# Kernel optimization log

Measured on AMD Instinct MI355X. Metric: run time of the kernel, lower is better.

The kernel has to match this reference:

```python
import jax, jax.numpy as jnp
import numpy as np
from jax import lax

B, S, D, N, K = 4, 8192, 128, 2, 3
G = N + 1  # n_order + 1 projection groups
EPS_L1 = 1e-8


def _theta(d):
    # RoPE inverse frequencies: 10000^{-2i/d}
    return 1.0 / (10000.0 ** (jnp.arange(d // 2, dtype=jnp.float32) * 2.0 / d))


def _rope(x, pos, theta):
    # x: (B,S,D), pos: (B,S) int -> dimension-wise 2x2 rotations
    ang = pos[..., None].astype(jnp.float32) * theta  # (B,S,D/2)
    c, s = jnp.cos(ang), jnp.sin(ang)
    xe, xo = x[..., 0::2], x[..., 1::2]
    return jnp.stack([xe * c - xo * s, xe * s + xo * c], axis=-1).reshape(x.shape)


def _layernorm(x, g, b, eps=1e-5):
    mu = jnp.mean(x, axis=-1, keepdims=True)
    var = jnp.var(x, axis=-1, keepdims=True)
    return (x - mu) / jnp.sqrt(var + eps) * g + b


def _fft_long_conv(v, h):
    # torch norm='forward': rfft divides by n, irfft does not -> circular conv / (2L)
    L = v.shape[-1]
    n = 2 * L
    V = jnp.fft.rfft(v, n=n, norm='forward')
    H = jnp.fft.rfft(h, n=n, norm='forward')
    return jnp.fft.irfft(V * H, n=n, norm='forward')[..., :L]


def setup_inputs() -> dict:
    key = jax.random.key(0)
    ks = jax.random.split(key, 8)
    sc = lambda fan_in: (2.0 / fan_in) ** 0.5
    return {
        'embeddings': jax.random.normal(ks[0], (B, S, D), dtype=jnp.float32),
        'W_proj': jax.random.normal(ks[1], (D, G * D), dtype=jnp.float32) * sc(D),
        'conv_w': jax.random.normal(ks[2], (G * D, 1, K), dtype=jnp.float32) * sc(K),
        'conv_b': jnp.zeros((G * D,), dtype=jnp.float32),
        'W1': jax.random.normal(ks[3], (D, D), dtype=jnp.float32) * sc(D),
        'b1': jnp.zeros((D,), dtype=jnp.float32),
        'ln_g': jnp.ones((D,), dtype=jnp.float32),
        'ln_b': jnp.zeros((D,), dtype=jnp.float32),
        'W2': jax.random.normal(ks[4], (D, N * D), dtype=jnp.float32) * sc(D),
        'b2': jnp.zeros((N * D,), dtype=jnp.float32),
        'ff_scale': jnp.ones((1, 1, N * D), dtype=jnp.float32),
        'out_proj': jax.random.normal(ks[5], (D, D), dtype=jnp.float32) * sc(D),
        'B_param': jax.random.normal(ks[6], (N, 1, D, 1), dtype=jnp.float32) * sc(D),
        'positions': (jnp.arange(B * S, dtype=jnp.int32).reshape(B, S) % S),
    }


def reference(embeddings, W_proj, conv_w, conv_b, W1, b1, ln_g, ln_b, W2, b2,
              ff_scale, out_proj, B_param, positions):
    theta = _theta(D)
    # --- HyenaProjection: dense proj + fully-depthwise short conv ---
    x = embeddings @ W_proj                      # (B,S,G*D)
    xc = jnp.transpose(x, (0, 2, 1))             # (B,G*D,S)
    z = lax.conv_general_dilated(
        xc, conv_w, (1,), [(K // 2, K // 2)],
        dimension_numbers=('NCH', 'OIH', 'NCH'),
        feature_group_count=G * D) + conv_b[None, :, None]
    # faithful to torch: (B,S,G*D) row-major reshape into (B,D,G,S)
    z = jnp.transpose(z, (0, 2, 1)).reshape(B, D, G, S)
    z_list = [z[:, :, i, :] for i in range(G)]   # each (B,D,S)
    # --- HyenaFilter: RoPE + FFN + L1 normalization over emb dim ---
    t = _rope(embeddings, positions, theta)
    hmid = jax.nn.gelu(_layernorm(t @ W1 + b1, ln_g, ln_b), approximate=False)
    h_hat = (hmid @ W2 + b2) * ff_scale          # (B,S,N*D)
    h_hat = jnp.transpose(h_hat.reshape(B, S, N, D), (0, 2, 3, 1))  # (B,N,D,S)
    h_hat = h_hat / (jnp.sum(jnp.abs(h_hat), axis=-2, keepdims=True) + EPS_L1)
    # --- Hyena recurrence with FFT long conv ---
    v = z_list[-1]
    for i in range(N):
        v = z_list[i] * (_fft_long_conv(v, h_hat[:, i]) + B_param[i] * v)
    out = jnp.transpose(v, (0, 2, 1)) @ out_proj  # (B,S,D)
    return out
```

## Files before the change

kernel.cpp:

```cpp
#include <hip/hip_runtime.h>
#include <hip/hip_bf16.h>
#include <cstdint>

#define BB 4
#define SS 8192
#define DD 128

#define N_EMB  4194304
#define N_WP   49152
#define N_CW   1152
#define N_CB   384
#define N_W1   16384
#define N_B1   128
#define N_LNG  128
#define N_LNB  128
#define N_W2   32768
#define N_B2   256
#define N_FFS  256
#define N_WO   16384
#define N_BP   256
#define N_FINP 4311680

__device__ __forceinline__ void bfsplit(float v, unsigned short& h, unsigned short& l)
{
    __hip_bfloat16 hb = __float2bfloat16(v);
    float hf = __bfloat162float(hb);
    __hip_bfloat16 lb = __float2bfloat16(v - hf);
    h = *(unsigned short*)&hb;
    l = *(unsigned short*)&lb;
}

struct SrcPtrs { const void* p[13]; };

__global__ __launch_bounds__(256) void k_convert(
    SrcPtrs sp, float* __restrict__ dst,
    unsigned short* __restrict__ embh, unsigned short* __restrict__ embl,
    unsigned short* __restrict__ wpth, unsigned short* __restrict__ wptl)
{
    static const int sizes[13] = {N_EMB, N_WP, N_CW, N_CB, N_W1, N_B1, N_LNG,
                                  N_LNB, N_W2, N_B2, N_FFS, N_WO, N_BP};
    const unsigned probe = *(const unsigned*)sp.p[6];
    const bool isbf = (probe != 0x3F800000u);
    const int gid = blockIdx.x * 256 + threadIdx.x;
    const int stride = gridDim.x * 256;
    int off = 0;
    for (int seg = 0; seg < 13; ++seg) {
        const int n = sizes[seg];
        float* d = dst + off;
        if (isbf) {
            const unsigned short* s = (const unsigned short*)sp.p[seg];
            for (int i = gid; i < n; i += stride) {
                float v = __uint_as_float(((unsigned)s[i]) << 16);
                d[i] = v;
                if (seg == 0) { unsigned short h, l; bfsplit(v, h, l); embh[i] = h; embl[i] = l; }
            }
        } else {
            const float* s = (const float*)sp.p[seg];
            for (int i = gid; i < n; i += stride) {
                float v = s[i];
                d[i] = v;
                if (seg == 0) { unsigned short h, l; bfsplit(v, h, l); embh[i] = h; embl[i] = l; }
            }
        }
        off += n;
    }
    for (int i = gid; i < N_WP; i += stride) {
        int n = i >> 7, k = i & 127;
        float v;
        if (isbf) v = __uint_as_float(((unsigned)((const unsigned short*)sp.p[1])[k * 384 + n]) << 16);
        else      v = ((const float*)sp.p[1])[k * 384 + n];
        unsigned short h, l; bfsplit(v, h, l);
        wpth[i] = h; wptl[i] = l;
    }
}

#define PCROWS 112

__global__ __launch_bounds__(512) void k_projconv(
    const unsigned short* __restrict__ embh,
    const unsigned short* __restrict__ embl,
    const unsigned short* __restrict__ wpth,
    const unsigned short* __restrict__ wptl,
    const float* __restrict__ cw,
    const float* __restrict__ cb,
    float* __restrict__ zbuf)
{
    typedef short bf16x8 __attribute__((ext_vector_type(8)));
    typedef float f32x4 __attribute__((ext_vector_type(4)));
    __shared__ float xs[128][68];

    const int b    = blockIdx.y;
    const int s0   = blockIdx.x * PCROWS;
    const int t    = threadIdx.x;
    const int wv   = t >> 6;
    const int lane = t & 63;
    const int m    = lane & 15;
    const int q    = lane >> 4;

    bf16x8 Ah[4], Al[4];
    {
        int sx  = s0 - 8 + 16 * wv + m;
        int sxc = min(max(sx, 0), SS - 1);
        const size_t rowoff = ((size_t)b * SS + sxc) * DD;
        #pragma unroll
        for (int kt = 0; kt < 4; ++kt) {
            int k0 = kt * 32 + q * 8;
            Ah[kt] = *(const bf16x8*)(embh + rowoff + k0);
            Al[kt] = *(const bf16x8*)(embl + rowoff + k0);
        }
    }

    for (int nc = 0; nc < 6; ++nc) {
        #pragma unroll
        for (int nt = 0; nt < 4; ++nt) {
            int n = nc * 64 + nt * 16 + m;
            const size_t noff = (size_t)n * DD;
            f32x4 acc = {0.f, 0.f, 0.f, 0.f};
            #pragma unroll
            for (int kt = 0; kt < 4; ++kt) {
                int k0 = kt * 32 + q * 8;
                bf16x8 Bh = *(const bf16x8*)(wpth + noff + k0);
                bf16x8 Bl = *(const bf16x8*)(wptl + noff + k0);
                acc = __builtin_amdgcn_mfma_f32_16x16x32_bf16(Ah[kt], Bh, acc, 0, 0, 0);
                acc = __builtin_amdgcn_mfma_f32_16x16x32_bf16(Ah[kt], Bl, acc, 0, 0, 0);
                acc = __builtin_amdgcn_mfma_f32_16x16x32_bf16(Al[kt], Bh, acc, 0, 0, 0);
            }
            #pragma unroll
            for (int rg = 0; rg < 4; ++rg)
                xs[16 * wv + 4 * q + rg][nt * 16 + m] = acc[rg];
        }
        __syncthreads();
        {
            int c = t & 63, rg = t >> 6;
            int ch = nc * 64 + c;
            float w0 = cw[ch * 3 + 0], w1 = cw[ch * 3 + 1], w2 = cw[ch * 3 + 2];
            float bias = cb[ch];
            #pragma unroll
            for (int i = 0; i < 14; ++i) {
                int r = rg + 8 * i;
                int s = s0 + r;
                if (s < SS) {
                    float x0 = (s > 0)      ? xs[r + 7][c] : 0.f;
                    float x1 = xs[r + 8][c];
                    float x2 = (s < SS - 1) ? xs[r + 9][c] : 0.f;
                    zbuf[((size_t)b * SS + s) * 384 + ch] = x0 * w0 + x1 * w1 + x2 * w2 + bias;
                }
            }
        }
        __syncthreads();
    }
}

__global__ __launch_bounds__(256) void k_mlp(
    const float* __restrict__ emb,
    const int* __restrict__ positions,
    const float* __restrict__ W1,
    const float* __restrict__ b1,
    const float* __restrict__ ln_g,
    const float* __restrict__ ln_b,
    const float* __restrict__ W2,
    const float* __restrict__ b2,
    const float* __restrict__ ffs,
    float* __restrict__ hhat)
{
    const int b  = blockIdx.y;
    const int s0 = blockIdx.x * 16;
    const int t  = threadIdx.x;
    __shared__ float tls[16][128];
    __shared__ float hls[16][128];
    __shared__ float hh[16][257];
    __shared__ float rstat[16][2];

    for (int idx = t; idx < 16 * 64; idx += 256) {
        int r = idx >> 6, i = idx & 63;
        int s = s0 + r;
        const float2 p = ((const float2*)(emb + ((size_t)b * SS + s) * DD))[i];
        float xe = p.x, xo = p.y;
        float pos = (float)positions[(size_t)b * SS + s];
        float th = exp2f((float)i * (-13.287712379549449f / 64.0f));
        float ang = pos * th;
        float sn, cs;
        sincosf(ang, &sn, &cs);
        tls[r][2 * i]     = xe * cs - xo * sn;
        tls[r][2 * i + 1] = xe * sn + xo * cs;
    }
    __syncthreads();

    {
        const int jc = t & 127;
        const int rbase = t >> 7;
        float bias = b1[jc];
        float acc[8];
        #pragma unroll
        for (int ri = 0; ri < 8; ++ri) acc[ri] = bias;
        for (int k = 0; k < 128; ++k) {
            float wv = W1[k * 128 + jc];
            #pragma unroll
            for (int ri = 0; ri < 8; ++ri)
                acc[ri] += tls[rbase + 2 * ri][k] * wv;
        }
        #pragma unroll
        for (int ri = 0; ri < 8; ++ri) hls[rbase + 2 * ri][jc] = acc[ri];
    }
    __syncthreads();

    {
        const int wave = t >> 6, lane = t & 63;
        for (int r = wave; r < 16; r += 4) {
            float x0 = hls[r][lane], x1 = hls[r][lane + 64];
            float sum = x0 + x1, ssq = x0 * x0 + x1 * x1;
            #pragma unroll
            for (int off = 32; off > 0; off >>= 1) {
                sum += __shfl_xor(sum, off);
                ssq += __shfl_xor(ssq, off);
            }
            float mu  = sum * (1.0f / 128.0f);
            float var = ssq * (1.0f / 128.0f) - mu * mu;
            float inv = rsqrtf(var + 1e-5f);
            float y0 = (x0 - mu) * inv * ln_g[lane]      + ln_b[lane];
            float y1 = (x1 - mu) * inv * ln_g[lane + 64] + ln_b[lane + 64];
            hls[r][lane]      = y0 * 0.5f * (1.0f + erff(y0 * 0.70710678118654752f));
            hls[r][lane + 64] = y1 * 0.5f * (1.0f + erff(y1 * 0.70710678118654752f));
        }
    }
    __syncthreads();

    {
        const int jc = t;
        float acc[16];
        #pragma unroll
        for (int ri = 0; ri < 16; ++ri) acc[ri] = 0.f;
        for (int k = 0; k < 128; ++k) {
            float wv = W2[k * 256 + jc];
            #pragma unroll
            for (int ri = 0; ri < 16; ++ri)
                acc[ri] += hls[ri][k] * wv;
        }
        float bias = b2[jc];
        float fsc  = ffs[jc];
        #pragma unroll
        for (int ri = 0; ri < 16; ++ri)
            hh[ri][jc] = (acc[ri] + bias) * fsc;
    }
    __syncthreads();

    {
        const int wave = t >> 6, lane = t & 63;
        for (int g = wave; g < 32; g += 4) {
            int r = g >> 1, n = g & 1;
            float a = fabsf(hh[r][n * 128 + lane]) + fabsf(hh[r][n * 128 + lane + 64]);
            #pragma unroll
            for (int off = 32; off > 0; off >>= 1) a += __shfl_xor(a, off);
            if (lane == 0) rstat[r][n] = 1.0f / (a + 1e-8f);
        }
    }
    __syncthreads();

    for (int idx = t; idx < 16 * 256; idx += 256) {
        int nd = idx >> 4, rr = idx & 15;
        int n = nd >> 7;
        float val = hh[rr][nd] * rstat[rr][n];
        hhat[((size_t)(b * 2 + n) * 128 + (nd & 127)) * SS + (s0 + rr)] = val;
    }
}

__device__ __forceinline__ int SK(int x) { return x + (x >> 5); }

__global__ __launch_bounds__(1024) void k_fftconv(
    const float* __restrict__ zbuf,
    const float* __restrict__ hhat,
    const float* __restrict__ Bp,
    float* __restrict__ vout)
{
    const int d = blockIdx.x;
    const int b = blockIdx.y;
    const int t = threadIdx.x;
    __shared__ float lre[4224];
    __shared__ float lim[4224];
    __shared__ float2 twF[1280];

    const float c8 = 0.923879532511287f, s8 = 0.382683432365090f, c4 = 0.707106781186548f;

    {
        const int lhs_c[5] = {9, 7, 5, 3, 1};
        for (int idx = t; idx < 1280; idx += 1024) {
            int si = idx >> 8, jj = idx & 255;
            float sn, cs;
            sincospif((float)jj * (-1.0f / (float)(1 << lhs_c[si])), &sn, &cs);
            twF[idx] = make_float2(cs, sn);
        }
    }

    const float* zb = zbuf + (size_t)b * (SS * 384);
    const float* v0 = zb + ((size_t)d * 3 + 2) * SS;
    float vr[8];
    #pragma unroll
    for (int j = 0; j < 8; ++j) vr[j] = v0[t + j * 1024];

    float cre[16], cim[16];
    const float sc = 1.0f / 536870912.0f;
    const int blk = t >> 8, w = t & 255;
    __syncthreads();

    for (int it = 0; it < 2; ++it) {
        const float* hp = hhat + (((size_t)b * 2 + it) * 128 + d) * SS;
        #pragma unroll
        for (int j = 0; j < 8; ++j) { cre[j] = vr[j]; cim[j] = hp[t + j * 1024]; }

        {
            float W0i, W0r; sincospif((float)t * (-1.0f / 8192.0f), &W0i, &W0r);
            const float wjr[4] = {1.f, c8, c4, s8};
            const float wji[4] = {0.f, -s8, -c4, -c8};
            #pragma unroll
            for (int j = 0; j < 4; ++j) {
                float Wr = W0r * wjr[j] - W0i * wji[j];
                float Wi = W0r * wji[j] + W0i * wjr[j];
                float W2r = Wr * Wr - Wi * Wi, W2i = 2.f * Wr * Wi;
                float W3r = W2r * Wr - W2i * Wi, W3i = W2r * Wi + W2i * Wr;
                float a0r = cre[j], a0i = cim[j], a1r = cre[j + 4], a1i = cim[j + 4];
                cre[j] = a0r + a1r; cim[j] = a0i + a1i;
                float dr = a0r - a1r, di = a0i - a1i;
                cre[j + 4] = W2r * dr - W2i * di; cim[j + 4] = W2r * di + W2i * dr;
                float e2r = a0r + a1i, e2i = a0i - a1r;
                cre[j + 8] = Wr * e2r - Wi * e2i; cim[j + 8] = Wr * e2i + Wi * e2r;
                float e3r = a0r - a1i, e3i = a0i + a1r;
                cre[j + 12] = W3r * e3r - W3i * e3i; cim[j + 12] = W3r * e3i + W3i * e3r;
            }
        }
        {
            float Wi, Wr; sincospif((float)t * (-1.0f / 2048.0f), &Wi, &Wr);
            float W2r = Wr * Wr - Wi * Wi, W2i = 2.f * Wr * Wi;
            float W3r = W2r * Wr - W2i * Wi, W3i = W2r * Wi + W2i * Wr;
            #pragma unroll
            for (int g = 0; g < 16; g += 4) {
                float a0r = cre[g], a0i = cim[g], a1r = cre[g + 1], a1i = cim[g + 1];
                float a2r = cre[g + 2], a2i = cim[g + 2], a3r = cre[g + 3], a3i = cim[g + 3];
                float s02r = a0r + a2r, s02i = a0i + a2i, d02r = a0r - a2r, d02i = a0i - a2i;
                float s13r = a1r + a3r, s13i = a1i + a3i, d13r = a1r - a3r, d13i = a1i - a3i;
                cre[g] = s02r + s13r; cim[g] = s02i + s13i;
                float u1r = s02r - s13r, u1i = s02i - s13i;
                cre[g + 1] = W2r * u1r - W2i * u1i; cim[g + 1] = W2r * u1i + W2i * u1r;
                float e2r = d02r + d13i, e2i = d02i - d13r;
                cre[g + 2] = Wr * e2r - Wi * e2i; cim[g + 2] = Wr * e2i + Wi * e2r;
                float e3r = d02r - d13i, e3i = d02i + d13r;
                cre[g + 3] = W3r * e3r - W3i * e3i; cim[g + 3] = W3r * e3i + W3i * e3r;
            }
        }
        #pragma unroll
        for (int p = 0; p < 4; ++p) {
            #pragma unroll
            for (int q = 0; q < 4; ++q) {
                int a = SK(q * 1024 + t);
                lre[a] = cre[4 * p + q]; lim[a] = cim[4 * p + q];
            }
            __syncthreads();
            const int lhs_c[5] = {9, 7, 5, 3, 1};
            #pragma unroll
            for (int si = 0; si < 5; ++si) {
                const int lh = lhs_c[si];
                const int hh = 1 << lh, h2 = hh >> 1;
                const int jj = w & (h2 - 1);
                const int i0 = blk * 1024 + ((w >> (lh - 1)) << (lh + 1)) + jj;
                const float2 wv = twF[si * 256 + jj];
                const float Wr = wv.x, Wi = wv.y;
                const int p0 = SK(i0), p1 = SK(i0 + h2), p2 = SK(i0 + hh), p3 = SK(i0 + hh + h2);
                float a0r = lre[p0], a0i = lim[p0];
                float a1r = lre[p1], a1i = lim[p1];
                float a2r = lre[p2], a2i = lim[p2];
                float a3r = lre[p3], a3i = lim[p3];
                float W2r = Wr * Wr - Wi * Wi, W2i = 2.f * Wr * Wi;
                float W3r = W2r * Wr - W2i * Wi, W3i = W2r * Wi + W2i * Wr;
                float s02r = a0r + a2r, s02i = a0i + a2i, d02r = a0r - a2r, d02i = a0i - a2i;
                float s13r = a1r + a3r, s13i = a1i + a3i, d13r = a1r - a3r, d13i = a1i - a3i;
                lre[p0] = s02r + s13r; lim[p0] = s02i + s13i;
                float u1r = s02r - s13r, u1i = s02i - s13i;
                lre[p1] = W2r * u1r - W2i * u1i; lim[p1] = W2r * u1i + W2i * u1r;
                float e2r = d02r + d13i, e2i = d02i - d13r;
                lre[p2] = Wr * e2r - Wi * e2i; lim[p2] = Wr * e2i + Wi * e2r;
                float e3r = d02r - d13i, e3i = d02i + d13r;
                lre[p3] = W3r * e3r - W3i * e3i; lim[p3] = W3r * e3i + W3i * e3r;
                __syncthreads();
            }
            #pragma unroll
            for (int q = 0; q < 4; ++q) {
                int a = SK(q * 1024 + t);
                cre[4 * p + q] = lre[a]; cim[4 * p + q] = lim[a];
            }
            __syncthreads();
        }

        #pragma unroll
        for (int j = 0; j < 16; ++j) {
            float Cr = cre[j], Ci = cim[j];
            cre[j] = (Cr * Cr - Ci * Ci) * sc;
            cim[j] = 2.0f * Cr * Ci * sc;
        }

        #pragma unroll
        for (int p = 0; p < 4; ++p) {
            #pragma unroll
            for (int q = 0; q < 4; ++q) {
                int a = SK(q * 1024 + t);
                lre[a] = cre[4 * p + q]; lim[a] = cim[4 * p + q];
            }
            __syncthreads();
            const int lqs_c[5] = {0, 2, 4, 6, 8};
            #pragma unroll
            for (int si = 0; si < 5; ++si) {
                const int lq = lqs_c[si];
                const int qv = 1 << lq;
                const int jj = w & (qv - 1);
                const int i0 = blk * 1024 + ((w >> lq) << (lq + 2)) + jj;
                const float2 wv = twF[(4 - si) * 256 + jj];
                const float Wbr = wv.x, Wbi = -wv.y;
                const int p0 = SK(i0), p1 = SK(i0 + qv), p2 = SK(i0 + 2 * qv), p3 = SK(i0 + 3 * qv);
                float a0r = lre[p0], a0i = lim[p0];
                float a1r = lre[p1], a1i = lim[p1];
                float a2r = lre[p2], a2i = lim[p2];
                float a3r = lre[p3], a3i = lim[p3];
                float War = Wbr * Wbr - Wbi * Wbi, Wai = 2.f * Wbr * Wbi;
                float t1r = War * a1r - Wai * a1i, t1i = War * a1i + Wai * a1r;
                float b0r = a0r + t1r, b0i = a0i + t1i, b1r = a0r - t1r, b1i = a0i - t1i;
                float t3r = War * a3r - Wai * a3i, t3i = War * a3i + Wai * a3r;
                float b2r = a2r + t3r, b2i = a2i + t3i, b3r = a2r - t3r, b3i = a2i - t3i;
                float u2r = Wbr * b2r - Wbi * b2i, u2i = Wbr * b2i + Wbi * b2r;
                lre[p0] = b0r + u2r; lim[p0] = b0i + u2i;
                lre[p2] = b0r - u2r; lim[p2] = b0i - u2i;
                float u3r = -Wbi * b3r - Wbr * b3i, u3i = Wbr * b3r - Wbi * b3i;
                lre[p1] = b1r + u3r; lim[p1] = b1i + u3i;
                lre[p3] = b1r - u3r; lim[p3] = b1i - u3i;
                __syncthreads();
            }
            #pragma unroll
            for (int q = 0; q < 4; ++q) {
                int a = SK(q * 1024 + t);
                cre[4 * p + q] = lre[a]; cim[4 * p + q] = lim[a];
            }
            __syncthreads();
        }
        {
            float Wbi, Wbr; sincospif((float)t * (1.0f / 2048.0f), &Wbi, &Wbr);
            float War = Wbr * Wbr - Wbi * Wbi, Wai = 2.f * Wbr * Wbi;
            #pragma unroll
            for (int g = 0; g < 16; g += 4) {
                float a0r = cre[g], a0i = cim[g], a1r = cre[g + 1], a1i = cim[g + 1];
                float a2r = cre[g + 2], a2i = cim[g + 2], a3r = cre[g + 3], a3i = cim[g + 3];
                float t1r = War * a1r - Wai * a1i, t1i = War * a1i + Wai * a1r;
                float b0r = a0r + t1r, b0i = a0i + t1i, b1r = a0r - t1r, b1i = a0i - t1i;
                float t3r = War * a3r - Wai * a3i, t3i = War * a3i + Wai * a3r;
                float b2r = a2r + t3r, b2i = a2i + t3i, b3r = a2r - t3r, b3i = a2i - t3i;
                float u2r = Wbr * b2r - Wbi * b2i, u2i = Wbr * b2i + Wbi * b2r;
                cre[g] = b0r + u2r; cim[g] = b0i + u2i;
                cre[g + 2] = b0r - u2r; cim[g + 2] = b0i - u2i;
                float u3r = -Wbi * b3r - Wbr * b3i, u3i = Wbr * b3r - Wbi * b3i;
                cre[g + 1] = b1r + u3r; cim[g + 1] = b1i + u3i;
                cre[g + 3] = b1r - u3r; cim[g + 3] = b1i - u3i;
            }
        }
        {
            float Bi, Br; sincospif((float)t * (1.0f / 8192.0f), &Bi, &Br);
            const float bjr[4] = {1.f, c8, c4, s8};
            const float bji[4] = {0.f, s8, c4, c8};
            #pragma unroll
            for (int j = 0; j < 4; ++j) {
                float Wbr = Br * bjr[j] - Bi * bji[j];
                float Wbi = Br * bji[j] + Bi * bjr[j];
                float War = Wbr * Wbr - Wbi * Wbi, Wai = 2.f * Wbr * Wbi;
                float a0r = cre[j], a0i = cim[j], a1r = cre[j + 4], a1i = cim[j + 4];
                float a2r = cre[j + 8], a2i = cim[j + 8], a3r = cre[j + 12], a3i = cim[j + 12];
                float t1r = War * a1r - Wai * a1i, t1i = War * a1i + Wai * a1r;
                float b0r = a0r + t1r, b0i = a0i + t1i, b1r = a0r - t1r, b1i = a0i - t1i;
                float t3r = War * a3r - Wai * a3i, t3i = War * a3i + Wai * a3r;
                float b2r = a2r + t3r, b2i = a2i + t3i, b3r = a2r - t3r, b3i = a2i - t3i;
                float u2r = Wbr * b2r - Wbi * b2i, u2i = Wbr * b2i + Wbi * b2r;
                cre[j] = b0r + u2r; cim[j] = b0i + u2i;
                cre[j + 8] = b0r - u2r; cim[j + 8] = b0i - u2i;
                float u3r = -Wbi * b3r - Wbr * b3i, u3i = Wbr * b3r - Wbi * b3i;
                cre[j + 4] = b1r + u3r; cim[j + 4] = b1i + u3i;
                cre[j + 12] = b1r - u3r; cim[j + 12] = b1i - u3i;
            }
        }

        const float* zi = zb + ((size_t)d * 3 + it) * SS;
        const float bpv = Bp[it * 128 + d];
        #pragma unroll
        for (int j = 0; j < 8; ++j) {
            float zz = zi[t + j * 1024];
            vr[j] = zz * (cim[j] + bpv * vr[j]);
        }
        __syncthreads();
    }

    float* vo = vout + ((size_t)b * 128 + d) * SS;
    #pragma unroll
    for (int j = 0; j < 8; ++j) vo[t + j * 1024] = vr[j];
}

__global__ __launch_bounds__(256) void k_outproj(
    const float* __restrict__ vbuf,
    const float* __restrict__ Wo,
    const unsigned* __restrict__ probe,
    void* __restrict__ outv)
{
    const int b  = blockIdx.y;
    const int s0 = blockIdx.x * 64;
    const int t  = threadIdx.x;
    __shared__ float vt[128 * 64];
    for (int idx = t; idx < 8192; idx += 256) {
        int dd = idx >> 6, sl = idx & 63;
        vt[idx] = vbuf[((size_t)b * 128 + dd) * SS + s0 + sl];
    }
    const bool isbf = (*probe != 0x3F800000u);
    __syncthreads();
    {
        const int jc  = t & 127;
        const int slb = t >> 7;
        float acc[32];
        #pragma unroll
        for (int ii = 0; ii < 32; ++ii) acc[ii] = 0.f;
        for (int k = 0; k < 128; ++k) {
            float wv = Wo[k * 128 + jc];
            #pragma unroll
            for (int ii = 0; ii < 32; ++ii)
                acc[ii] += vt[k * 64 + slb + 2 * ii] * wv;
        }
        if (isbf) {
            __hip_bfloat16* out = (__hip_bfloat16*)outv;
            #pragma unroll
            for (int ii = 0; ii < 32; ++ii)
                out[((size_t)b * SS + s0 + slb + 2 * ii) * DD + jc] = __float2bfloat16(acc[ii]);
        } else {
            float* out = (float*)outv;
            #pragma unroll
            for (int ii = 0; ii < 32; ++ii)
                out[((size_t)b * SS + s0 + slb + 2 * ii) * DD + jc] = acc[ii];
        }
    }
}

extern "C" void kernel_launch(void* const* d_in, const int* in_sizes, int n_in,
                              void* d_out, int out_size, void* d_ws, size_t ws_size,
                              hipStream_t stream)
{
    (void)in_sizes; (void)n_in; (void)out_size; (void)ws_size;
    const int* positions = (const int*)d_in[13];

    float* finp = (float*)d_ws;
    float* zbuf = finp + N_FINP;
    float* hhat = zbuf + (size_t)BB * SS * 384;
    float* vbuf = hhat + (size_t)BB * 2 * 128 * SS;
    unsigned short* embh = (unsigned short*)(vbuf + (size_t)BB * 128 * SS);
    unsigned short* embl = embh + N_EMB;
    unsigned short* wpth = embl + N_EMB;
    unsigned short* wptl = wpth + N_WP;

    const float* emb = finp;
    const float* Wp  = emb + N_EMB;
    const float* cw  = Wp  + N_WP;
    const float* cb  = cw  + N_CW;
    const float* W1  = cb  + N_CB;
    const float* b1  = W1  + N_W1;
    const float* lng = b1  + N_B1;
    const float* lnb = lng + N_LNG;
    const float* W2  = lnb + N_LNB;
    const float* b2  = W2  + N_W2;
    const float* ffs = b2  + N_B2;
    const float* Wo  = ffs + N_FFS;
    const float* Bp  = Wo  + N_WO;

    SrcPtrs sp;
    for (int i = 0; i < 13; ++i) sp.p[i] = d_in[i];

    k_convert<<<dim3(2048), 256, 0, stream>>>(sp, finp, embh, embl, wpth, wptl);
    k_projconv<<<dim3((SS + PCROWS - 1) / PCROWS, BB), 512, 0, stream>>>(
        embh, embl, wpth, wptl, cw, cb, zbuf);
    k_mlp<<<dim3(SS / 16, BB), 256, 0, stream>>>(emb, positions, W1, b1, lng, lnb, W2, b2, ffs, hhat);
    k_fftconv<<<dim3(DD, BB), 1024, 0, stream>>>(zbuf, hhat, Bp, vbuf);
    k_outproj<<<dim3(SS / 64, BB), 256, 0, stream>>>(vbuf, Wo, (const unsigned*)d_in[6], d_out);
}
```

Before: 491.0 us.

## Move MLP and output projection GEMMs onto split-bf16 MFMA

Replaces the scalar fp32 FMA loops for W1, W2 and out_proj with 16x16x32 bf16 MFMA instructions. Activations and weights are split into hi/lo bf16 parts and three MFMAs are issued per tile to keep roughly fp32 accuracy. The convert kernel now also writes transposed hi/lo copies of the three weights. Shared-memory tiles are padded to cut bank conflicts. This adds conversion work and some precision risk, in exchange for much higher matrix throughput in k_mlp and k_outproj.

```diff
diff --git a/kernel.cpp b/kernel.cpp
--- a/kernel.cpp
+++ b/kernel.cpp
@@ -21,6 +21,9 @@
 #define N_BP   256
 #define N_FINP 4311680
 
+typedef short bf16x8 __attribute__((ext_vector_type(8)));
+typedef float f32x4  __attribute__((ext_vector_type(4)));
+
 __device__ __forceinline__ void bfsplit(float v, unsigned short& h, unsigned short& l)
 {
     __hip_bfloat16 hb = __float2bfloat16(v);
@@ -30,12 +33,33 @@
     l = *(unsigned short*)&lb;
 }
 
+__device__ __forceinline__ void packAB(const float* __restrict__ src, bf16x8& H, bf16x8& L)
+{
+    float4 x0 = *(const float4*)(src);
+    float4 x1 = *(const float4*)(src + 4);
+    float xv[8] = {x0.x, x0.y, x0.z, x0.w, x1.x, x1.y, x1.z, x1.w};
+    unsigned short h[8], l[8];
+    #pragma unroll
+    for (int j = 0; j < 8; ++j) bfsplit(xv[j], h[j], l[j]);
+    #pragma unroll
+    for (int j = 0; j < 8; ++j) { H[j] = (short)h[j]; L[j] = (short)l[j]; }
+}
+
 struct SrcPtrs { const void* p[13]; };
+
+__device__ __forceinline__ float readf(const void* p, int idx, bool isbf)
+{
+    if (isbf) return __uint_as_float(((unsigned)((const unsigned short*)p)[idx]) << 16);
+    return ((const float*)p)[idx];
+}
 
 __global__ __launch_bounds__(256) void k_convert(
     SrcPtrs sp, float* __restrict__ dst,
     unsigned short* __restrict__ embh, unsigned short* __restrict__ embl,
-    unsigned short* __restrict__ wpth, unsigned short* __restrict__ wptl)
+    unsigned short* __restrict__ wpth, unsigned short* __restrict__ wptl,
+    unsigned short* __restrict__ w1th, unsigned short* __restrict__ w1tl,
+    unsigned short* __restrict__ w2th, unsigned short* __restrict__ w2tl,
+    unsigned short* __restrict__ woth, unsigned short* __restrict__ wotl)
 {
     static const int sizes[13] = {N_EMB, N_WP, N_CW, N_CB, N_W1, N_B1, N_LNG,
                                   N_LNB, N_W2, N_B2, N_FFS, N_WO, N_BP};
@@ -47,30 +71,32 @@
     for (int seg = 0; seg < 13; ++seg) {
         const int n = sizes[seg];
         float* d = dst + off;
-        if (isbf) {
-            const unsigned short* s = (const unsigned short*)sp.p[seg];
-            for (int i = gid; i < n; i += stride) {
-                float v = __uint_as_float(((unsigned)s[i]) << 16);
-                d[i] = v;
-                if (seg == 0) { unsigned short h, l; bfsplit(v, h, l); embh[i] = h; embl[i] = l; }
-            }
-        } else {
-            const float* s = (const float*)sp.p[seg];
-            for (int i = gid; i < n; i += stride) {
-                float v = s[i];
-                d[i] = v;
-                if (seg == 0) { unsigned short h, l; bfsplit(v, h, l); embh[i] = h; embl[i] = l; }
-            }
+        for (int i = gid; i < n; i += stride) {
+            float v = readf(sp.p[seg], i, isbf);
+            d[i] = v;
+            if (seg == 0) { unsigned short h, l; bfsplit(v, h, l); embh[i] = h; embl[i] = l; }
         }
         off += n;
     }
     for (int i = gid; i < N_WP; i += stride) {
         int n = i >> 7, k = i & 127;
-        float v;
-        if (isbf) v = __uint_as_float(((unsigned)((const unsigned short*)sp.p[1])[k * 384 + n]) << 16);
-        else      v = ((const float*)sp.p[1])[k * 384 + n];
-        unsigned short h, l; bfsplit(v, h, l);
+        unsigned short h, l; bfsplit(readf(sp.p[1], k * 384 + n, isbf), h, l);
         wpth[i] = h; wptl[i] = l;
+    }
+    for (int i = gid; i < N_W1; i += stride) {
+        int n = i >> 7, k = i & 127;
+        unsigned short h, l; bfsplit(readf(sp.p[4], k * 128 + n, isbf), h, l);
+        w1th[i] = h; w1tl[i] = l;
+    }
+    for (int i = gid; i < N_W2; i += stride) {
+        int n = i >> 7, k = i & 127;
+        unsigned short h, l; bfsplit(readf(sp.p[8], k * 256 + n, isbf), h, l);
+        w2th[i] = h; w2tl[i] = l;
+    }
+    for (int i = gid; i < N_WO; i += stride) {
+        int n = i >> 7, k = i & 127;
+        unsigned short h, l; bfsplit(readf(sp.p[11], k * 128 + n, isbf), h, l);
+        woth[i] = h; wotl[i] = l;
     }
 }
 
@@ -85,8 +111,6 @@
     const float* __restrict__ cb,
     float* __restrict__ zbuf)
 {
-    typedef short bf16x8 __attribute__((ext_vector_type(8)));
-    typedef float f32x4 __attribute__((ext_vector_type(4)));
     __shared__ float xs[128][68];
 
     const int b    = blockIdx.y;
@@ -154,11 +178,13 @@
 __global__ __launch_bounds__(256) void k_mlp(
     const float* __restrict__ emb,
     const int* __restrict__ positions,
-    const float* __restrict__ W1,
+    const unsigned short* __restrict__ w1th,
+    const unsigned short* __restrict__ w1tl,
     const float* __restrict__ b1,
     const float* __restrict__ ln_g,
     const float* __restrict__ ln_b,
-    const float* __restrict__ W2,
+    const unsigned short* __restrict__ w2th,
+    const unsigned short* __restrict__ w2tl,
     const float* __restrict__ b2,
     const float* __restrict__ ffs,
     float* __restrict__ hhat)
@@ -166,8 +192,8 @@
     const int b  = blockIdx.y;
     const int s0 = blockIdx.x * 16;
     const int t  = threadIdx.x;
-    __shared__ float tls[16][128];
-    __shared__ float hls[16][128];
+    __shared__ float tls[16][132];
+    __shared__ float hls[16][132];
     __shared__ float hh[16][257];
     __shared__ float rstat[16][2];
 
@@ -186,27 +212,38 @@
     }
     __syncthreads();
 
+    const int wv = t >> 6, lane = t & 63, m = lane & 15, q = lane >> 4;
+
     {
-        const int jc = t & 127;
-        const int rbase = t >> 7;
-        float bias = b1[jc];
-        float acc[8];
-        #pragma unroll
-        for (int ri = 0; ri < 8; ++ri) acc[ri] = bias;
-        for (int k = 0; k < 128; ++k) {
-            float wv = W1[k * 128 + jc];
-            #pragma unroll
-            for (int ri = 0; ri < 8; ++ri)
-                acc[ri] += tls[rbase + 2 * ri][k] * wv;
-        }
-        #pragma unroll
-        for (int ri = 0; ri < 8; ++ri) hls[rbase + 2 * ri][jc] = acc[ri];
+        bf16x8 Ah[4], Al[4];
+        #pragma unroll
+        for (int kt = 0; kt < 4; ++kt)
+            packAB(&tls[m][kt * 32 + q * 8], Ah[kt], Al[kt]);
+        #pragma unroll
+        for (int ntl = 0; ntl < 2; ++ntl) {
+            int nt = 2 * wv + ntl;
+            int col = nt * 16 + m;
+            const size_t noff = (size_t)col * 128;
+            f32x4 acc = {0.f, 0.f, 0.f, 0.f};
+            #pragma unroll
+            for (int kt = 0; kt < 4; ++kt) {
+                int k0 = kt * 32 + q * 8;
+                bf16x8 Bh = *(const bf16x8*)(w1th + noff + k0);
+                bf16x8 Bl = *(const bf16x8*)(w1tl + noff + k0);
+                acc = __builtin_amdgcn_mfma_f32_16x16x32_bf16(Ah[kt], Bh, acc, 0, 0, 0);
+                acc = __builtin_amdgcn_mfma_f32_16x16x32_bf16(Ah[kt], Bl, acc, 0, 0, 0);
+                acc = __builtin_amdgcn_mfma_f32_16x16x32_bf16(Al[kt], Bh, acc, 0, 0, 0);
+            }
+            float bias = b1[col];
+            #pragma unroll
+            for (int rg = 0; rg < 4; ++rg)
+                hls[4 * q + rg][col] = acc[rg] + bias;
+        }
     }
     __syncthreads();
 
     {
-        const int wave = t >> 6, lane = t & 63;
-        for (int r = wave; r < 16; r += 4) {
+        for (int r = wv; r < 16; r += 4) {
             float x0 = hls[r][lane], x1 = hls[r][lane + 64];
             float sum = x0 + x1, ssq = x0 * x0 + x1 * x1;
             #pragma unroll
@@ -226,27 +263,36 @@
     __syncthreads();
 
     {
-        const int jc = t;
-        float acc[16];
-        #pragma unroll
-        for (int ri = 0; ri < 16; ++ri) acc[ri] = 0.f;
-        for (int k = 0; k < 128; ++k) {
-            float wv = W2[k * 256 + jc];
-            #pragma unroll
-            for (int ri = 0; ri < 16; ++ri)
-                acc[ri] += hls[ri][k] * wv;
-        }
-        float bias = b2[jc];
-        float fsc  = ffs[jc];
-        #pragma unroll
-        for (int ri = 0; ri < 16; ++ri)
-            hh[ri][jc] = (acc[ri] + bias) * fsc;
+        bf16x8 Ah[4], Al[4];
+        #pragma unroll
+        for (int kt = 0; kt < 4; ++kt)
+            packAB(&hls[m][kt * 32 + q * 8], Ah[kt], Al[kt]);
+        #pragma unroll
+        for (int ntl = 0; ntl < 4; ++ntl) {
+            int nt = 4 * wv + ntl;
+            int col = nt * 16 + m;
+            const size_t noff = (size_t)col * 128;
+            f32x4 acc = {0.f, 0.f, 0.f, 0.f};
+            #pragma unroll
+            for (int kt = 0; kt < 4; ++kt) {
+                int k0 = kt * 32 + q * 8;
+                bf16x8 Bh = *(const bf16x8*)(w2th + noff + k0);
+                bf16x8 Bl = *(const bf16x8*)(w2tl + noff + k0);
+                acc = __builtin_amdgcn_mfma_f32_16x16x32_bf16(Ah[kt], Bh, acc, 0, 0, 0);
+                acc = __builtin_amdgcn_mfma_f32_16x16x32_bf16(Ah[kt], Bl, acc, 0, 0, 0);
+                acc = __builtin_amdgcn_mfma_f32_16x16x32_bf16(Al[kt], Bh, acc, 0, 0, 0);
+            }
+            float bias = b2[col];
+            float fsc  = ffs[col];
+            #pragma unroll
+            for (int rg = 0; rg < 4; ++rg)
+                hh[4 * q + rg][col] = (acc[rg] + bias) * fsc;
+        }
     }
     __syncthreads();
 
     {
-        const int wave = t >> 6, lane = t & 63;
-        for (int g = wave; g < 32; g += 4) {
+        for (int g = wv; g < 32; g += 4) {
             int r = g >> 1, n = g & 1;
             float a = fabsf(hh[r][n * 128 + lane]) + fabsf(hh[r][n * 128 + lane + 64]);
             #pragma unroll
@@ -498,43 +544,74 @@
 
 __global__ __launch_bounds__(256) void k_outproj(
     const float* __restrict__ vbuf,
-    const float* __restrict__ Wo,
+    const unsigned short* __restrict__ woth,
+    const unsigned short* __restrict__ wotl,
     const unsigned* __restrict__ probe,
     void* __restrict__ outv)
 {
+    __shared__ float vt[128 * 65];
     const int b  = blockIdx.y;
     const int s0 = blockIdx.x * 64;
     const int t  = threadIdx.x;
-    __shared__ float vt[128 * 64];
     for (int idx = t; idx < 8192; idx += 256) {
         int dd = idx >> 6, sl = idx & 63;
-        vt[idx] = vbuf[((size_t)b * 128 + dd) * SS + s0 + sl];
+        vt[dd * 65 + sl] = vbuf[((size_t)b * 128 + dd) * SS + s0 + sl];
     }
     const bool isbf = (*probe != 0x3F800000u);
     __syncthreads();
-    {
-        const int jc  = t & 127;
-        const int slb = t >> 7;
-        float acc[32];
-        #pragma unroll
-        for (int ii = 0; ii < 32; ++ii) acc[ii] = 0.f;
-        for (int k = 0; k < 128; ++k) {
-            float wv = Wo[k * 128 + jc];
-            #pragma unroll
-            for (int ii = 0; ii < 32; ++ii)
-                acc[ii] += vt[k * 64 + slb + 2 * ii] * wv;
-        }
-        if (isbf) {
-            __hip_bfloat16* out = (__hip_bfloat16*)outv;
-            #pragma unroll
-            for (int ii = 0; ii < 32; ++ii)
-                out[((size_t)b * SS + s0 + slb + 2 * ii) * DD + jc] = __float2bfloat16(acc[ii]);
-        } else {
-            float* out = (float*)outv;
-            #pragma unroll
-            for (int ii = 0; ii < 32; ++ii)
-                out[((size_t)b * SS + s0 + slb + 2 * ii) * DD + jc] = acc[ii];
-        }
+
+    const int wv = t >> 6, lane = t & 63, m = lane & 15, q = lane >> 4;
+
+    bf16x8 Ah[4], Al[4];
+    #pragma unroll
+    for (int kt = 0; kt < 4; ++kt) {
+        float xv[8];
+        unsigned short h[8], l[8];
+        #pragma unroll
+        for (int j = 0; j < 8; ++j) {
+            int dd = kt * 32 + q * 8 + j;
+            xv[j] = vt[dd * 65 + 16 * wv + m];
+        }
+        #pragma unroll
+        for (int j = 0; j < 8; ++j) bfsplit(xv[j], h[j], l[j]);
+        #pragma unroll
+        for (int j = 0; j < 8; ++j) { Ah[kt][j] = (short)h[j]; Al[kt][j] = (short)l[j]; }
+    }
+
+    f32x4 acc[8];
+    #pragma unroll
+    for (int nt = 0; nt < 8; ++nt) {
+        acc[nt] = (f32x4){0.f, 0.f, 0.f, 0.f};
+        const size_t noff = (size_t)(nt * 16 + m) * 128;
+        #pragma unroll
+        for (int kt = 0; kt < 4; ++kt) {
+            int k0 = kt * 32 + q * 8;
+            bf16x8 Bh = *(const bf16x8*)(woth + noff + k0);
+            bf16x8 Bl = *(const bf16x8*)(wotl + noff + k0);
+            acc[nt] = __builtin_amdgcn_mfma_f32_16x16x32_bf16(Ah[kt], Bh, acc[nt], 0, 0, 0);
+            acc[nt] = __builtin_amdgcn_mfma_f32_16x16x32_bf16(Ah[kt], Bl, acc[nt], 0, 0, 0);
+            acc[nt] = __builtin_amdgcn_mfma_f32_16x16x32_bf16(Al[kt], Bh, acc[nt], 0, 0, 0);
+        }
+    }
+
+    if (isbf) {
+        __hip_bfloat16* out = (__hip_bfloat16*)outv;
+        #pragma unroll
+        for (int nt = 0; nt < 8; ++nt)
+            #pragma unroll
+            for (int rg = 0; rg < 4; ++rg) {
+                int s = s0 + 16 * wv + 4 * q + rg;
+                out[((size_t)b * SS + s) * DD + nt * 16 + m] = __float2bfloat16(acc[nt][rg]);
+            }
+    } else {
+        float* out = (float*)outv;
+        #pragma unroll
+        for (int nt = 0; nt < 8; ++nt)
+            #pragma unroll
+            for (int rg = 0; rg < 4; ++rg) {
+                int s = s0 + 16 * wv + 4 * q + rg;
+                out[((size_t)b * SS + s) * DD + nt * 16 + m] = acc[nt][rg];
+            }
     }
 }
 
@@ -553,28 +630,33 @@
     unsigned short* embl = embh + N_EMB;
     unsigned short* wpth = embl + N_EMB;
     unsigned short* wptl = wpth + N_WP;
+    unsigned short* w1th = wptl + N_WP;
+    unsigned short* w1tl = w1th + N_W1;
+    unsigned short* w2th = w1tl + N_W1;
+    unsigned short* w2tl = w2th + N_W2;
+    unsigned short* woth = w2tl + N_W2;
+    unsigned short* wotl = woth + N_WO;
 
     const float* emb = finp;
-    const float* Wp  = emb + N_EMB;
-    const float* cw  = Wp  + N_WP;
+    const float* cw  = finp + N_EMB + N_WP;
     const float* cb  = cw  + N_CW;
-    const float* W1  = cb  + N_CB;
-    const float* b1  = W1  + N_W1;
+    const float* b1  = cb  + N_CB + N_W1;
     const float* lng = b1  + N_B1;
     const float* lnb = lng + N_LNG;
-    const float* W2  = lnb + N_LNB;
-    const float* b2  = W2  + N_W2;
+    const float* b2  = lnb + N_LNB + N_W2;
     const float* ffs = b2  + N_B2;
-    const float* Wo  = ffs + N_FFS;
-    const float* Bp  = Wo  + N_WO;
+    const float* Bp  = ffs + N_FFS + N_WO;
 
     SrcPtrs sp;
     for (int i = 0; i < 13; ++i) sp.p[i] = d_in[i];
 
-    k_convert<<<dim3(2048), 256, 0, stream>>>(sp, finp, embh, embl, wpth, wptl);
+    k_convert<<<dim3(2048), 256, 0, stream>>>(sp, finp, embh, embl, wpth, wptl,
+                                              w1th, w1tl, w2th, w2tl, woth, wotl);
     k_projconv<<<dim3((SS + PCROWS - 1) / PCROWS, BB), 512, 0, stream>>>(
         embh, embl, wpth, wptl, cw, cb, zbuf);
-    k_mlp<<<dim3(SS / 16, BB), 256, 0, stream>>>(emb, positions, W1, b1, lng, lnb, W2, b2, ffs, hhat);
+    k_mlp<<<dim3(SS / 16, BB), 256, 0, stream>>>(emb, positions, w1th, w1tl, b1,
+                                                 lng, lnb, w2th, w2tl, b2, ffs, hhat);
     k_fftconv<<<dim3(DD, BB), 1024, 0, stream>>>(zbuf, hhat, Bp, vbuf);
-    k_outproj<<<dim3(SS / 64, BB), 256, 0, stream>>>(vbuf, Wo, (const unsigned*)d_in[6], d_out);
-}
+    k_outproj<<<dim3(SS / 64, BB), 256, 0, stream>>>(vbuf, woth, wotl,
+                                                     (const unsigned*)d_in[6], d_out);
+}
```

Measured after the change: 412.1 us, median of 2. -16.1%, faster.
